# Kernel optimization log

Hardware: AMD Instinct MI355X
Metric: run time of the kernel (lower is better)

Reference implementation:

```python
import jax, jax.numpy as jnp
import numpy as np

NUM_EXPERTS = 8
TOP_K = 2
N_EMBD = 1024
D_FFN = 2048  # 4*N_EMBD // TOP_K, already multiple of BLOCK_N=128
BLOCK_M = 128
NORM_TOPK = True


def setup_inputs() -> dict:
    key = jax.random.key(0)
    k1, k2, k3 = jax.random.split(key, 3)
    x = jax.random.normal(k1, (2, 2048, N_EMBD), dtype=jnp.float32)
    router_w = jax.random.normal(k2, (NUM_EXPERTS, N_EMBD), dtype=jnp.float32) * 0.02
    w1 = jax.random.normal(k3, (N_EMBD, D_FFN * NUM_EXPERTS), dtype=jnp.float32) * 0.02
    return {"x": x, "router_w": router_w, "w1": w1}


def reference(x, router_w, w1):
    B, S, H = x.shape
    x_flat = x.reshape(-1, H)                                   # [T, H]
    router_logits = x_flat @ router_w.T                         # [T, E]
    probs = jax.nn.softmax(router_logits.astype(jnp.float32), axis=-1)
    rweights, sel = jax.lax.top_k(probs, TOP_K)                 # [T, k]
    if NORM_TOPK:
        rweights = rweights / rweights.sum(axis=-1, keepdims=True)
    rweights = rweights.astype(x.dtype)

    # repeat_interleave tokens top_k times, then stable-sort by expert id
    x_rep = jnp.repeat(x_flat, TOP_K, axis=0)                   # [M, H]
    sel_rep = sel.reshape(-1)                                   # [M]
    rw_rep = rweights.reshape(-1, 1)                            # [M, 1]
    order = jnp.argsort(sel_rep, stable=True)                   # expert-sort permutation
    x_grouped = x_rep[order]                                    # [M, H]
    sel_sorted = sel_rep[order]                                 # [M]
    rw_sorted = rw_rep[order]                                   # [M, 1]

    M = x_grouped.shape[0]
    nblk = M // BLOCK_M                                         # M divisible by BLOCK_M by construction
    # SDD kernel: expert of the first row of each BLOCK_M block selects w1 slice
    block_expert = sel_sorted[::BLOCK_M]                        # [nblk] == col_indices_ptr
    w1e = w1.reshape(H, NUM_EXPERTS, D_FFN)                     # w1[:, e*D:(e+1)*D] == w1e[:, e, :]
    w_blk = jnp.take(w1e, block_expert, axis=1)                 # [H, nblk, D]
    x_blk = x_grouped.reshape(nblk, BLOCK_M, H)                 # [nblk, Bm, H]
    block_sparse = jnp.einsum('bmh,hbd->bmd', x_blk, w_blk).reshape(M, D_FFN)

    block_sparse = jax.nn.gelu(block_sparse, approximate=False) * rw_sorted
    return block_sparse, router_logits
```

## Files before the change

### kernel.cpp

```cpp
#include <hip/hip_runtime.h>
#include <hip/hip_bf16.h>
#include <cmath>

typedef float f32x4 __attribute__((ext_vector_type(4)));
typedef __bf16 bf16x8 __attribute__((ext_vector_type(8)));
typedef __bf16 bf16x4 __attribute__((ext_vector_type(4)));

#define NE 8
#define H 1024
#define DF 2048
#define WCOLS 16384
#define NTOK 4096
#define MROWS 8192
#define NBLK 64

typedef const __attribute__((address_space(1))) unsigned int glb_u32;
typedef __attribute__((address_space(3))) unsigned int lds_u32;

__device__ __forceinline__ void async_load16(const void* g, void* l) {
    __builtin_amdgcn_global_load_lds((glb_u32*)g, (lds_u32*)l, 16, 0, 0);
}

__global__ __launch_bounds__(256) void router_kernel(
    const float* __restrict__ x, const float* __restrict__ rw,
    float* __restrict__ logits, int* __restrict__ sel, float* __restrict__ rwn,
    __bf16* __restrict__ xb)
{
    int gid  = blockIdx.x * blockDim.x + threadIdx.x;
    int tok  = gid >> 6;
    int lane = gid & 63;
    const float* xr = x + (size_t)tok * H;
    __bf16* xbr = xb + (size_t)tok * H;
    float acc[NE];
#pragma unroll
    for (int e = 0; e < NE; ++e) acc[e] = 0.f;
#pragma unroll
    for (int it = 0; it < 4; ++it) {
        int k = (it * 64 + lane) * 4;
        float4 xv = *(const float4*)(xr + k);
        bf16x4 xc;
        xc[0] = (__bf16)xv.x; xc[1] = (__bf16)xv.y;
        xc[2] = (__bf16)xv.z; xc[3] = (__bf16)xv.w;
        *(bf16x4*)(xbr + k) = xc;
#pragma unroll
        for (int e = 0; e < NE; ++e) {
            float4 wv = *(const float4*)(rw + e * H + k);
            acc[e] += xv.x * wv.x + xv.y * wv.y + xv.z * wv.z + xv.w * wv.w;
        }
    }
#pragma unroll
    for (int e = 0; e < NE; ++e) {
        float v = acc[e];
#pragma unroll
        for (int off = 32; off > 0; off >>= 1) v += __shfl_xor(v, off, 64);
        acc[e] = v;
    }
    if (lane == 0) {
#pragma unroll
        for (int e = 0; e < NE; ++e) logits[tok * NE + e] = acc[e];
        int i1 = 0; float m1 = acc[0];
#pragma unroll
        for (int e = 1; e < NE; ++e) if (acc[e] > m1) { m1 = acc[e]; i1 = e; }
        int i2 = -1; float m2 = -INFINITY;
#pragma unroll
        for (int e = 0; e < NE; ++e) if (e != i1 && acc[e] > m2) { m2 = acc[e]; i2 = e; }
        float e2 = expf(m2 - m1);
        float inv = 1.f / (1.f + e2);
        sel[tok * 2]     = i1;  sel[tok * 2 + 1] = i2;
        rwn[tok * 2]     = inv; rwn[tok * 2 + 1] = e2 * inv;
    }
}

__global__ __launch_bounds__(256) void transpose_w(
    const float* __restrict__ w1, __bf16* __restrict__ w1t)
{
    __shared__ float tile[64][65];
    int kb = blockIdx.x * 64;
    int nb = blockIdx.y * 64;
    int t  = threadIdx.x;
    int kk = t >> 4;
    int nn = (t & 15) * 4;
#pragma unroll
    for (int r = 0; r < 4; ++r) {
        int k = kk + r * 16;
        float4 v = *(const float4*)(w1 + (size_t)(kb + k) * WCOLS + nb + nn);
        tile[k][nn]     = v.x;
        tile[k][nn + 1] = v.y;
        tile[k][nn + 2] = v.z;
        tile[k][nn + 3] = v.w;
    }
    __syncthreads();
    int n_local = t >> 2;
    int kc = (t & 3) * 16;
    bf16x8 o0, o1;
#pragma unroll
    for (int i = 0; i < 8; ++i) {
        o0[i] = (__bf16)tile[kc + i][n_local];
        o1[i] = (__bf16)tile[kc + 8 + i][n_local];
    }
    __bf16* dst = w1t + (size_t)(nb + n_local) * H + kb + kc;
    *(bf16x8*)dst       = o0;
    *(bf16x8*)(dst + 8) = o1;
}

__global__ __launch_bounds__(256) void sort_kernel(
    const int* __restrict__ sel, const float* __restrict__ rwn,
    int* __restrict__ stok, float* __restrict__ srw, int* __restrict__ bexp)
{
    __shared__ int cnt[NE][256];
    __shared__ int tot[NE];
    __shared__ int ebase[NE + 1];
    int t = threadIdx.x;
    int selv[32];
    int lc[NE];
#pragma unroll
    for (int e = 0; e < NE; ++e) lc[e] = 0;
    int base = t * 32;
    for (int j = 0; j < 32; ++j) { selv[j] = sel[base + j]; lc[selv[j]]++; }
#pragma unroll
    for (int e = 0; e < NE; ++e) cnt[e][t] = lc[e];
    __syncthreads();
    {
        int g = t >> 5, j = t & 31;
        int s = 0, pre[8];
#pragma unroll
        for (int i = 0; i < 8; ++i) { pre[i] = s; s += cnt[g][j * 8 + i]; }
        int inc = s;
#pragma unroll
        for (int d = 1; d < 32; d <<= 1) {
            int v = __shfl_up(inc, d, 64);
            if (j >= d) inc += v;
        }
        int excl = inc - s;
#pragma unroll
        for (int i = 0; i < 8; ++i) cnt[g][j * 8 + i] = excl + pre[i];
        if (j == 31) tot[g] = inc;
    }
    __syncthreads();
    if (t == 0) {
        int s = 0;
        for (int e = 0; e < NE; ++e) { ebase[e] = s; s += tot[e]; }
        ebase[NE] = s;
    }
    __syncthreads();
    int off[NE];
#pragma unroll
    for (int e = 0; e < NE; ++e) off[e] = ebase[e] + cnt[e][t];
    for (int j = 0; j < 32; ++j) {
        int i = base + j;
        int e = selv[j];
        int pos = off[e]++;
        stok[pos] = i >> 1;
        srw[pos]  = rwn[i];
    }
    __syncthreads();
    if (t < NBLK) {
        int r = t * 128;
        int e = 0;
        while (e < NE - 1 && r >= ebase[e + 1]) ++e;
        bexp[t] = e;
    }
}

__global__ __launch_bounds__(256) void moe_gemm(
    const __bf16* __restrict__ xb, const __bf16* __restrict__ w1t,
    const int* __restrict__ stok, const float* __restrict__ srw,
    const int* __restrict__ bexp, float* __restrict__ out)
{
    __shared__ __align__(16) __bf16 As[128 * 32];
    __shared__ __align__(16) __bf16 Bs[128 * 32];
    __shared__ int   tokS[128];
    __shared__ float rwS[128];

    int bx = blockIdx.x;
    int by = blockIdx.y;
    int tid = threadIdx.x;
    int e = bexp[by];

    if (tid < 128) {
        tokS[tid] = stok[by * 128 + tid];
        rwS[tid]  = srw[by * 128 + tid];
    }
    __syncthreads();

    int lane = tid & 63;
    int wv   = tid >> 6;
    int rsub = lane >> 2;
    int kc   = (lane & 3) * 8;
    int r0   = wv * 32 + rsub;
    int r1   = r0 + 16;

    const char* aP0 = (const char*)(xb + (size_t)tokS[r0] * H + kc);
    const char* aP1 = (const char*)(xb + (size_t)tokS[r1] * H + kc);
    const __bf16* wbase = w1t + ((size_t)e * DF + (size_t)bx * 128) * H;
    const char* bP0 = (const char*)(wbase + (size_t)r0 * H + kc);
    const char* bP1 = (const char*)(wbase + (size_t)r1 * H + kc);
    __bf16* lA = As + wv * 1024;
    __bf16* lB = Bs + wv * 1024;

    int wm   = (wv & 1) * 64;
    int wn   = (wv >> 1) * 64;
    int quad = lane >> 4;
    int l16  = lane & 15;
    int kf   = quad * 8;

    f32x4 acc[4][4];
#pragma unroll
    for (int i = 0; i < 4; ++i)
#pragma unroll
        for (int j = 0; j < 4; ++j) acc[i][j] = (f32x4){0.f, 0.f, 0.f, 0.f};

    for (int k0 = 0; k0 < H; k0 += 32) {
        async_load16(aP0, lA);
        async_load16(aP1, lA + 512);
        async_load16(bP0, lB);
        async_load16(bP1, lB + 512);
        aP0 += 64; aP1 += 64; bP0 += 64; bP1 += 64;
        __syncthreads();

        bf16x8 af[4], bfr[4];
#pragma unroll
        for (int i = 0; i < 4; ++i)
            af[i] = *(const bf16x8*)&As[(wm + i * 16 + l16) * 32 + kf];
#pragma unroll
        for (int j = 0; j < 4; ++j)
            bfr[j] = *(const bf16x8*)&Bs[(wn + j * 16 + l16) * 32 + kf];
#pragma unroll
        for (int i = 0; i < 4; ++i)
#pragma unroll
            for (int j = 0; j < 4; ++j)
                acc[i][j] = __builtin_amdgcn_mfma_f32_16x16x32_bf16(
                    af[i], bfr[j], acc[i][j], 0, 0, 0);
        __syncthreads();
    }

#pragma unroll
    for (int i = 0; i < 4; ++i) {
#pragma unroll
        for (int r = 0; r < 4; ++r) {
            int m = wm + i * 16 + quad * 4 + r;
            float rwv = rwS[m];
            size_t orow = (size_t)(by * 128 + m) * DF + bx * 128;
#pragma unroll
            for (int j = 0; j < 4; ++j) {
                float val = acc[i][j][r];
                float g = 0.5f * val * (1.f + erff(val * 0.70710678118654752f));
                out[orow + wn + j * 16 + l16] = g * rwv;
            }
        }
    }
}

extern "C" void kernel_launch(void* const* d_in, const int* in_sizes, int n_in,
                              void* d_out, int out_size, void* d_ws, size_t ws_size,
                              hipStream_t stream) {
    (void)in_sizes; (void)n_in; (void)out_size; (void)ws_size;
    const float* x        = (const float*)d_in[0];
    const float* router_w = (const float*)d_in[1];
    const float* w1       = (const float*)d_in[2];
    float* out    = (float*)d_out;
    float* logits = out + (size_t)MROWS * DF;

    char* ws    = (char*)d_ws;
    int*   sel  = (int*)(ws);
    float* rwn  = (float*)(ws + 32768);
    int*   stok = (int*)(ws + 65536);
    float* srw  = (float*)(ws + 98304);
    int*   bexp = (int*)(ws + 131072);
    __bf16* xb  = (__bf16*)(ws + (1 << 20));
    __bf16* w1t = (__bf16*)(ws + (9 << 20));

    router_kernel<<<NTOK / 4, 256, 0, stream>>>(x, router_w, logits, sel, rwn, xb);
    transpose_w<<<dim3(16, 256), 256, 0, stream>>>(w1, w1t);
    sort_kernel<<<1, 256, 0, stream>>>(sel, rwn, stok, srw, bexp);
    moe_gemm<<<dim3(16, NBLK), 256, 0, stream>>>(xb, w1t, stok, srw, bexp, out);
}
```

Baseline: 215.1 us.

## Fuse router and weight prep, pre-tile weights, double-buffer 32x32 MFMA GEMM

The router and weight-transpose kernels are merged into one launch, and the weight is rewritten in a pre-tiled layout so each K-step's B tile is one contiguous 8KB chunk. The sort kernel now uses 1024 threads with a two-level scan. The GEMM switches to 32x32x16 MFMA, double-buffers its LDS tiles through async global-to-LDS loads with one barrier per step, and remaps block indices for better reuse. The exact erf GELU is replaced with a tanh approximation built on __expf, which may change numerics relative to the reference.

```diff
diff --git a/kernel.cpp b/kernel.cpp
--- a/kernel.cpp
+++ b/kernel.cpp
@@ -2,7 +2,7 @@
 #include <hip/hip_bf16.h>
 #include <cmath>
 
-typedef float f32x4 __attribute__((ext_vector_type(4)));
+typedef float f32x16 __attribute__((ext_vector_type(16)));
 typedef __bf16 bf16x8 __attribute__((ext_vector_type(8)));
 typedef __bf16 bf16x4 __attribute__((ext_vector_type(4)));
 
@@ -13,6 +13,7 @@
 #define NTOK 4096
 #define MROWS 8192
 #define NBLK 64
+#define TILE_E 4096
 
 typedef const __attribute__((address_space(1))) unsigned int glb_u32;
 typedef __attribute__((address_space(3))) unsigned int lds_u32;
@@ -21,134 +22,132 @@
     __builtin_amdgcn_global_load_lds((glb_u32*)g, (lds_u32*)l, 16, 0, 0);
 }
 
-__global__ __launch_bounds__(256) void router_kernel(
+__global__ __launch_bounds__(256) void prep_kernel(
     const float* __restrict__ x, const float* __restrict__ rw,
+    const float* __restrict__ w1,
     float* __restrict__ logits, int* __restrict__ sel, float* __restrict__ rwn,
-    __bf16* __restrict__ xb)
+    __bf16* __restrict__ xb, __bf16* __restrict__ Wt)
 {
-    int gid  = blockIdx.x * blockDim.x + threadIdx.x;
-    int tok  = gid >> 6;
-    int lane = gid & 63;
-    const float* xr = x + (size_t)tok * H;
-    __bf16* xbr = xb + (size_t)tok * H;
-    float acc[NE];
-#pragma unroll
-    for (int e = 0; e < NE; ++e) acc[e] = 0.f;
-#pragma unroll
-    for (int it = 0; it < 4; ++it) {
-        int k = (it * 64 + lane) * 4;
-        float4 xv = *(const float4*)(xr + k);
-        bf16x4 xc;
-        xc[0] = (__bf16)xv.x; xc[1] = (__bf16)xv.y;
-        xc[2] = (__bf16)xv.z; xc[3] = (__bf16)xv.w;
-        *(bf16x4*)(xbr + k) = xc;
+    __shared__ float tile[32][132];
+    int b = blockIdx.x;
+    int tid = threadIdx.x;
+    if (b < 1024) {
+        int tok  = b * 4 + (tid >> 6);
+        int lane = tid & 63;
+        const float* xr = x + (size_t)tok * H;
+        __bf16* xbr = xb + (size_t)tok * H;
+        float acc[NE];
+#pragma unroll
+        for (int e = 0; e < NE; ++e) acc[e] = 0.f;
+#pragma unroll
+        for (int it = 0; it < 4; ++it) {
+            int k = (it * 64 + lane) * 4;
+            float4 xv = *(const float4*)(xr + k);
+            bf16x4 xc;
+            xc[0] = (__bf16)xv.x; xc[1] = (__bf16)xv.y;
+            xc[2] = (__bf16)xv.z; xc[3] = (__bf16)xv.w;
+            *(bf16x4*)(xbr + k) = xc;
+#pragma unroll
+            for (int e = 0; e < NE; ++e) {
+                float4 wv = *(const float4*)(rw + e * H + k);
+                acc[e] += xv.x * wv.x + xv.y * wv.y + xv.z * wv.z + xv.w * wv.w;
+            }
+        }
 #pragma unroll
         for (int e = 0; e < NE; ++e) {
-            float4 wv = *(const float4*)(rw + e * H + k);
-            acc[e] += xv.x * wv.x + xv.y * wv.y + xv.z * wv.z + xv.w * wv.w;
-        }
-    }
-#pragma unroll
-    for (int e = 0; e < NE; ++e) {
-        float v = acc[e];
-#pragma unroll
-        for (int off = 32; off > 0; off >>= 1) v += __shfl_xor(v, off, 64);
-        acc[e] = v;
-    }
-    if (lane == 0) {
-#pragma unroll
-        for (int e = 0; e < NE; ++e) logits[tok * NE + e] = acc[e];
-        int i1 = 0; float m1 = acc[0];
-#pragma unroll
-        for (int e = 1; e < NE; ++e) if (acc[e] > m1) { m1 = acc[e]; i1 = e; }
-        int i2 = -1; float m2 = -INFINITY;
-#pragma unroll
-        for (int e = 0; e < NE; ++e) if (e != i1 && acc[e] > m2) { m2 = acc[e]; i2 = e; }
-        float e2 = expf(m2 - m1);
-        float inv = 1.f / (1.f + e2);
-        sel[tok * 2]     = i1;  sel[tok * 2 + 1] = i2;
-        rwn[tok * 2]     = inv; rwn[tok * 2 + 1] = e2 * inv;
-    }
-}
-
-__global__ __launch_bounds__(256) void transpose_w(
-    const float* __restrict__ w1, __bf16* __restrict__ w1t)
-{
-    __shared__ float tile[64][65];
-    int kb = blockIdx.x * 64;
-    int nb = blockIdx.y * 64;
-    int t  = threadIdx.x;
-    int kk = t >> 4;
-    int nn = (t & 15) * 4;
-#pragma unroll
-    for (int r = 0; r < 4; ++r) {
-        int k = kk + r * 16;
-        float4 v = *(const float4*)(w1 + (size_t)(kb + k) * WCOLS + nb + nn);
-        tile[k][nn]     = v.x;
-        tile[k][nn + 1] = v.y;
-        tile[k][nn + 2] = v.z;
-        tile[k][nn + 3] = v.w;
-    }
-    __syncthreads();
-    int n_local = t >> 2;
-    int kc = (t & 3) * 16;
+            float v = acc[e];
+#pragma unroll
+            for (int off = 32; off > 0; off >>= 1) v += __shfl_xor(v, off, 64);
+            acc[e] = v;
+        }
+        if (lane == 0) {
+#pragma unroll
+            for (int e = 0; e < NE; ++e) logits[tok * NE + e] = acc[e];
+            int i1 = 0; float m1 = acc[0];
+#pragma unroll
+            for (int e = 1; e < NE; ++e) if (acc[e] > m1) { m1 = acc[e]; i1 = e; }
+            int i2 = -1; float m2 = -INFINITY;
+#pragma unroll
+            for (int e = 0; e < NE; ++e) if (e != i1 && acc[e] > m2) { m2 = acc[e]; i2 = e; }
+            float e2 = expf(m2 - m1);
+            float inv = 1.f / (1.f + e2);
+            sel[tok * 2]     = i1;  sel[tok * 2 + 1] = i2;
+            rwn[tok * 2]     = inv; rwn[tok * 2 + 1] = e2 * inv;
+        }
+        return;
+    }
+    int g  = b - 1024;
+    int c  = g >> 5;
+    int kb = g & 31;
+    int kk = tid >> 3;
+    int cc = (tid & 7) * 16;
+    const float* src = w1 + (size_t)(kb * 32 + kk) * WCOLS + c * 128 + cc;
+#pragma unroll
+    for (int i = 0; i < 4; ++i) {
+        float4 v = *(const float4*)(src + i * 4);
+        *(float4*)&tile[kk][cc + i * 4] = v;
+    }
+    __syncthreads();
+    int n = tid >> 1, kc0 = (tid & 1) * 16;
     bf16x8 o0, o1;
 #pragma unroll
     for (int i = 0; i < 8; ++i) {
-        o0[i] = (__bf16)tile[kc + i][n_local];
-        o1[i] = (__bf16)tile[kc + 8 + i][n_local];
-    }
-    __bf16* dst = w1t + (size_t)(nb + n_local) * H + kb + kc;
+        o0[i] = (__bf16)tile[kc0 + i][n];
+        o1[i] = (__bf16)tile[kc0 + 8 + i][n];
+    }
+    __bf16* dst = Wt + (size_t)g * TILE_E + n * 32 + kc0;
     *(bf16x8*)dst       = o0;
     *(bf16x8*)(dst + 8) = o1;
 }
 
-__global__ __launch_bounds__(256) void sort_kernel(
+__global__ __launch_bounds__(1024) void sort_kernel(
     const int* __restrict__ sel, const float* __restrict__ rwn,
     int* __restrict__ stok, float* __restrict__ srw, int* __restrict__ bexp)
 {
-    __shared__ int cnt[NE][256];
-    __shared__ int tot[NE];
+    __shared__ int cnt[NE][1024];
+    __shared__ int wtot[NE][2];
     __shared__ int ebase[NE + 1];
     int t = threadIdx.x;
-    int selv[32];
+    int selv[8];
     int lc[NE];
 #pragma unroll
     for (int e = 0; e < NE; ++e) lc[e] = 0;
-    int base = t * 32;
-    for (int j = 0; j < 32; ++j) { selv[j] = sel[base + j]; lc[selv[j]]++; }
+    int base = t * 8;
+#pragma unroll
+    for (int j = 0; j < 8; ++j) { selv[j] = sel[base + j]; lc[selv[j]]++; }
 #pragma unroll
     for (int e = 0; e < NE; ++e) cnt[e][t] = lc[e];
     __syncthreads();
-    {
-        int g = t >> 5, j = t & 31;
-        int s = 0, pre[8];
-#pragma unroll
-        for (int i = 0; i < 8; ++i) { pre[i] = s; s += cnt[g][j * 8 + i]; }
-        int inc = s;
-#pragma unroll
-        for (int d = 1; d < 32; d <<= 1) {
-            int v = __shfl_up(inc, d, 64);
-            if (j >= d) inc += v;
-        }
-        int excl = inc - s;
-#pragma unroll
-        for (int i = 0; i < 8; ++i) cnt[g][j * 8 + i] = excl + pre[i];
-        if (j == 31) tot[g] = inc;
-    }
+    int g = t >> 7, j = t & 127, jl = j & 63;
+    int s = 0, pre[8];
+#pragma unroll
+    for (int i = 0; i < 8; ++i) { pre[i] = s; s += cnt[g][j * 8 + i]; }
+    int inc = s;
+#pragma unroll
+    for (int d = 1; d < 64; d <<= 1) {
+        int v = __shfl_up(inc, d, 64);
+        if (jl >= d) inc += v;
+    }
+    if (jl == 63) wtot[g][j >> 6] = inc;
+    __syncthreads();
+    int add = (j >= 64) ? wtot[g][0] : 0;
+    int excl = inc - s + add;
+#pragma unroll
+    for (int i = 0; i < 8; ++i) cnt[g][j * 8 + i] = excl + pre[i];
     __syncthreads();
     if (t == 0) {
-        int s = 0;
-        for (int e = 0; e < NE; ++e) { ebase[e] = s; s += tot[e]; }
-        ebase[NE] = s;
+        int acc = 0;
+        for (int e = 0; e < NE; ++e) { ebase[e] = acc; acc += wtot[e][0] + wtot[e][1]; }
+        ebase[NE] = acc;
     }
     __syncthreads();
     int off[NE];
 #pragma unroll
     for (int e = 0; e < NE; ++e) off[e] = ebase[e] + cnt[e][t];
-    for (int j = 0; j < 32; ++j) {
-        int i = base + j;
-        int e = selv[j];
+#pragma unroll
+    for (int j2 = 0; j2 < 8; ++j2) {
+        int i = base + j2;
+        int e = selv[j2];
         int pos = off[e]++;
         stok[pos] = i >> 1;
         srw[pos]  = rwn[i];
@@ -162,93 +161,108 @@
     }
 }
 
-__global__ __launch_bounds__(256) void moe_gemm(
-    const __bf16* __restrict__ xb, const __bf16* __restrict__ w1t,
+__global__ __launch_bounds__(256, 4) void moe_gemm(
+    const __bf16* __restrict__ xb, const __bf16* __restrict__ Wt,
     const int* __restrict__ stok, const float* __restrict__ srw,
     const int* __restrict__ bexp, float* __restrict__ out)
 {
-    __shared__ __align__(16) __bf16 As[128 * 32];
-    __shared__ __align__(16) __bf16 Bs[128 * 32];
+    __shared__ __align__(16) __bf16 As[2][4096];
+    __shared__ __align__(16) __bf16 Bs[2][4096];
     __shared__ int   tokS[128];
     __shared__ float rwS[128];
 
-    int bx = blockIdx.x;
-    int by = blockIdx.y;
+    int g = blockIdx.x;
+    int by = (g & 7) * 8 + ((g >> 3) & 7);
+    int bx = g >> 6;
     int tid = threadIdx.x;
-    int e = bexp[by];
-
     if (tid < 128) {
         tokS[tid] = stok[by * 128 + tid];
         rwS[tid]  = srw[by * 128 + tid];
     }
+    int e = bexp[by];
     __syncthreads();
 
     int lane = tid & 63;
     int wv   = tid >> 6;
     int rsub = lane >> 2;
-    int kc   = (lane & 3) * 8;
+    int kcE  = (lane & 3) * 8;
     int r0   = wv * 32 + rsub;
     int r1   = r0 + 16;
 
-    const char* aP0 = (const char*)(xb + (size_t)tokS[r0] * H + kc);
-    const char* aP1 = (const char*)(xb + (size_t)tokS[r1] * H + kc);
-    const __bf16* wbase = w1t + ((size_t)e * DF + (size_t)bx * 128) * H;
-    const char* bP0 = (const char*)(wbase + (size_t)r0 * H + kc);
-    const char* bP1 = (const char*)(wbase + (size_t)r1 * H + kc);
-    __bf16* lA = As + wv * 1024;
-    __bf16* lB = Bs + wv * 1024;
-
-    int wm   = (wv & 1) * 64;
-    int wn   = (wv >> 1) * 64;
-    int quad = lane >> 4;
-    int l16  = lane & 15;
-    int kf   = quad * 8;
-
-    f32x4 acc[4][4];
-#pragma unroll
-    for (int i = 0; i < 4; ++i)
-#pragma unroll
-        for (int j = 0; j < 4; ++j) acc[i][j] = (f32x4){0.f, 0.f, 0.f, 0.f};
-
-    for (int k0 = 0; k0 < H; k0 += 32) {
-        async_load16(aP0, lA);
-        async_load16(aP1, lA + 512);
-        async_load16(bP0, lB);
-        async_load16(bP1, lB + 512);
-        aP0 += 64; aP1 += 64; bP0 += 64; bP1 += 64;
+    const __bf16* aS0 = xb + (size_t)tokS[r0] * H + kcE;
+    const __bf16* aS1 = xb + (size_t)tokS[r1] * H + kcE;
+    const __bf16* bT  = Wt + (size_t)(e * 16 + bx) * 32 * TILE_E + wv * 1024 + lane * 8;
+    __bf16* aL[2] = { &As[0][wv * 1024], &As[1][wv * 1024] };
+    __bf16* bL[2] = { &Bs[0][wv * 1024], &Bs[1][wv * 1024] };
+
+    int wm  = (wv & 1) * 64;
+    int wn  = (wv >> 1) * 64;
+    int l32 = lane & 31;
+    int khi = (lane >> 5) * 8;
+
+    f32x16 acc[2][2];
+#pragma unroll
+    for (int i = 0; i < 2; ++i)
+#pragma unroll
+        for (int j = 0; j < 2; ++j)
+#pragma unroll
+            for (int r = 0; r < 16; ++r) acc[i][j][r] = 0.f;
+
+    async_load16(aS0, aL[0]);
+    async_load16(aS1, aL[0] + 512);
+    async_load16(bT,  bL[0]);
+    async_load16(bT + 512, bL[0] + 512);
+
+    for (int kb = 0; kb < 32; ++kb) {
+        int cur = kb & 1;
         __syncthreads();
-
-        bf16x8 af[4], bfr[4];
-#pragma unroll
-        for (int i = 0; i < 4; ++i)
-            af[i] = *(const bf16x8*)&As[(wm + i * 16 + l16) * 32 + kf];
-#pragma unroll
-        for (int j = 0; j < 4; ++j)
-            bfr[j] = *(const bf16x8*)&Bs[(wn + j * 16 + l16) * 32 + kf];
-#pragma unroll
-        for (int i = 0; i < 4; ++i)
-#pragma unroll
-            for (int j = 0; j < 4; ++j)
-                acc[i][j] = __builtin_amdgcn_mfma_f32_16x16x32_bf16(
-                    af[i], bfr[j], acc[i][j], 0, 0, 0);
-        __syncthreads();
-    }
-
-#pragma unroll
-    for (int i = 0; i < 4; ++i) {
-#pragma unroll
-        for (int r = 0; r < 4; ++r) {
-            int m = wm + i * 16 + quad * 4 + r;
-            float rwv = rwS[m];
-            size_t orow = (size_t)(by * 128 + m) * DF + bx * 128;
-#pragma unroll
-            for (int j = 0; j < 4; ++j) {
-                float val = acc[i][j][r];
-                float g = 0.5f * val * (1.f + erff(val * 0.70710678118654752f));
-                out[orow + wn + j * 16 + l16] = g * rwv;
+        if (kb < 31) {
+            const __bf16* aN0 = aS0 + (kb + 1) * 32;
+            const __bf16* aN1 = aS1 + (kb + 1) * 32;
+            const __bf16* bN  = bT + (size_t)(kb + 1) * TILE_E;
+            async_load16(aN0, aL[1 - cur]);
+            async_load16(aN1, aL[1 - cur] + 512);
+            async_load16(bN,  bL[1 - cur]);
+            async_load16(bN + 512, bL[1 - cur] + 512);
+        }
+        bf16x8 af[2][2], bfr[2][2];
+#pragma unroll
+        for (int h = 0; h < 2; ++h) {
+#pragma unroll
+            for (int ti = 0; ti < 2; ++ti)
+                af[ti][h] = *(const bf16x8*)&As[cur][(wm + ti * 32 + l32) * 32 + h * 16 + khi];
+#pragma unroll
+            for (int tj = 0; tj < 2; ++tj)
+                bfr[tj][h] = *(const bf16x8*)&Bs[cur][(wn + tj * 32 + l32) * 32 + h * 16 + khi];
+        }
+#pragma unroll
+        for (int h = 0; h < 2; ++h)
+#pragma unroll
+            for (int ti = 0; ti < 2; ++ti)
+#pragma unroll
+                for (int tj = 0; tj < 2; ++tj)
+                    acc[ti][tj] = __builtin_amdgcn_mfma_f32_32x32x16_bf16(
+                        af[ti][h], bfr[tj][h], acc[ti][tj], 0, 0, 0);
+    }
+
+    int rowh = (lane >> 5) * 4;
+#pragma unroll
+    for (int ti = 0; ti < 2; ++ti)
+#pragma unroll
+        for (int tj = 0; tj < 2; ++tj)
+#pragma unroll
+            for (int reg = 0; reg < 16; ++reg) {
+                int row = (reg & 3) + 8 * (reg >> 2) + rowh;
+                int m = wm + ti * 32 + row;
+                int n = wn + tj * 32 + l32;
+                float val = acc[ti][tj][reg];
+                float u = 0.7978845608028654f * val * (1.f + 0.044715f * val * val);
+                float t = __expf(-2.f * fabsf(u));
+                float th = (1.f - t) / (1.f + t);
+                th = u < 0.f ? -th : th;
+                float gv = 0.5f * val * (1.f + th) * rwS[m];
+                out[(size_t)(by * 128 + m) * DF + bx * 128 + n] = gv;
             }
-        }
-    }
 }
 
 extern "C" void kernel_launch(void* const* d_in, const int* in_sizes, int n_in,
@@ -263,15 +277,14 @@
 
     char* ws    = (char*)d_ws;
     int*   sel  = (int*)(ws);
-    float* rwn  = (float*)(ws + 32768);
-    int*   stok = (int*)(ws + 65536);
-    float* srw  = (float*)(ws + 98304);
-    int*   bexp = (int*)(ws + 131072);
+    float* rwn  = (float*)(ws + 0x8000);
+    int*   stok = (int*)(ws + 0x10000);
+    float* srw  = (float*)(ws + 0x18000);
+    int*   bexp = (int*)(ws + 0x20000);
     __bf16* xb  = (__bf16*)(ws + (1 << 20));
-    __bf16* w1t = (__bf16*)(ws + (9 << 20));
-
-    router_kernel<<<NTOK / 4, 256, 0, stream>>>(x, router_w, logits, sel, rwn, xb);
-    transpose_w<<<dim3(16, 256), 256, 0, stream>>>(w1, w1t);
-    sort_kernel<<<1, 256, 0, stream>>>(sel, rwn, stok, srw, bexp);
-    moe_gemm<<<dim3(16, NBLK), 256, 0, stream>>>(xb, w1t, stok, srw, bexp, out);
-}
+    __bf16* Wt  = (__bf16*)(ws + (1 << 20) + (8 << 20));
+
+    prep_kernel<<<5120, 256, 0, stream>>>(x, router_w, w1, logits, sel, rwn, xb, Wt);
+    sort_kernel<<<1, 1024, 0, stream>>>(sel, rwn, stok, srw, bexp);
+    moe_gemm<<<16 * NBLK, 256, 0, stream>>>(xb, Wt, stok, srw, bexp, out);
+}
```

After: 189.1 us. -12.1%, faster.
